# Optimization experiments

Hardware: AMD Instinct MI355X
Metric: run time of the kernel (lower is better)

Reference implementation:

```python
import jax, jax.numpy as jnp
import numpy as np

N_NODES = 50000
N_EDGES = 800000
IN_CH, HID, OUT_CH, EDGE_DIM = 256, 128, 64, 64
NUM_LAYERS = 3


def _linear_init(key, fan_in, fan_out):
    # torch nn.Linear default: U(-1/sqrt(fan_in), 1/sqrt(fan_in))
    kw, kb = jax.random.split(key)
    bound = 1.0 / np.sqrt(fan_in)
    W = jax.random.uniform(kw, (fan_in, fan_out), minval=-bound, maxval=bound, dtype=jnp.float32)
    b = jax.random.uniform(kb, (fan_out,), minval=-bound, maxval=bound, dtype=jnp.float32)
    return W, b


def setup_inputs() -> dict:
    key = jax.random.key(0)
    ks = jax.random.split(key, 8)
    x = jax.random.normal(ks[0], (N_NODES, IN_CH), dtype=jnp.float32)
    edge_index = jax.random.randint(ks[1], (2, N_EDGES), 0, N_NODES, dtype=jnp.int64)
    edge_attr = jax.random.normal(ks[2], (N_EDGES, EDGE_DIM), dtype=jnp.float32)
    W_in, b_in = _linear_init(ks[3], IN_CH, HID)
    W_e, b_e = _linear_init(ks[4], EDGE_DIM, HID)
    W1, b1 = _linear_init(ks[5], HID, HID)
    W2, b2 = _linear_init(ks[6], HID, HID)
    W_out, b_out = _linear_init(ks[7], HID, OUT_CH)
    return {"x": x, "edge_index": edge_index, "edge_attr": edge_attr,
            "W_in": W_in, "b_in": b_in, "W_e": W_e, "b_e": b_e,
            "W1": W1, "b1": b1, "W2": W2, "b2": b2,
            "W_out": W_out, "b_out": b_out}


def reference(x, edge_index, edge_attr, W_in, b_in, W_e, b_e, W1, b1, W2, b2, W_out, b_out):
    N = x.shape[0]
    src, dst = edge_index[0], edge_index[1]
    # input projection (in_channels != hidden_channels)
    h = x @ W_in + b_in                      # [N, HID]
    # edge projection is layer-independent (shared GINEConv weights)
    e = edge_attr @ W_e + b_e                # [E, HID]
    for _ in range(NUM_LAYERS):
        # GINEConv: message = relu(h_src + e), sum-aggregate to dst, eps=0
        msg = jax.nn.relu(h[src] + e)        # [E, HID]
        agg = jax.ops.segment_sum(msg, dst, num_segments=N)
        z = h + agg                          # (1+eps)*h + agg, eps=0
        # conv nn: MLP Linear->relu->Linear (plain_last)
        z = jax.nn.relu(z @ W1 + b1) @ W2 + b2
        # outer act
        h = jax.nn.relu(z)
    return h @ W_out + b_out                 # [N, OUT_CH]
```

## Files before the change

### kernel.cpp

```cpp
#include <hip/hip_runtime.h>
#include <hip/hip_bf16.h>
#include <stdint.h>

#define N_NODES 50000
#define N_EDGES 800000
#define IN_CH 256
#define HID 128
#define OUT_CH 64
#define EDGE_DIM 64

typedef __hip_bfloat16 bf16;
typedef __attribute__((ext_vector_type(8))) short short8;
typedef __attribute__((ext_vector_type(4))) float f32x4;

__device__ __forceinline__ void st_out(float* p, float v) { *p = v; }
__device__ __forceinline__ void st_out(bf16* p, float v) { *p = __float2bfloat16(v); }

__launch_bounds__(256)
__global__ void wt_prep(const float* __restrict__ W, bf16* __restrict__ Wt, int K, int N) {
    int i = blockIdx.x * 256 + threadIdx.x;
    if (i >= K * N) return;
    int n = i % N, k = i / N;
    Wt[n * K + k] = __float2bfloat16(W[i]);
}

template<int KTOT, int N, bool RELU, bool PERM, typename OutT>
__launch_bounds__(256)
__global__ void gemm_mfma(const float* __restrict__ A, const bf16* __restrict__ Wt,
                          const float* __restrict__ b, OutT* __restrict__ out,
                          int M, const int* __restrict__ operm) {
    constexpr int KC  = (KTOT >= 128) ? 128 : KTOT;
    constexpr int NCH = KTOT / KC;
    constexpr int KCP = KC + 8;
    constexpr int NT  = N / 16;
    __shared__ __align__(16) bf16 Ws[N * KCP];
    __shared__ __align__(16) bf16 As[64 * KCP];

    const int tid  = threadIdx.x;
    const int wave = tid >> 6;
    const int lane = tid & 63;
    const int quad = lane >> 4;
    const int l16  = lane & 15;
    const int base = blockIdx.x * 64;

    f32x4 acc[NT];
    #pragma unroll
    for (int i = 0; i < NT; i++) acc[i] = (f32x4){0.f, 0.f, 0.f, 0.f};

    for (int ch = 0; ch < NCH; ch++) {
        const int kc = ch * KC;
        for (int t = tid * 4; t < N * KC; t += 256 * 4) {
            int n = t / KC, k = t % KC;
            *(uint2*)&Ws[n * KCP + k] = *(const uint2*)&Wt[n * KTOT + kc + k];
        }
        for (int t = tid * 4; t < 64 * KC; t += 256 * 4) {
            int r = t / KC, k = t % KC;
            int gr = base + r;
            float4 v = (gr < M) ? *(const float4*)&A[(size_t)gr * KTOT + kc + k]
                                : make_float4(0.f, 0.f, 0.f, 0.f);
            __hip_bfloat162 p0 = __float22bfloat162_rn(make_float2(v.x, v.y));
            __hip_bfloat162 p1 = __float22bfloat162_rn(make_float2(v.z, v.w));
            *(__hip_bfloat162*)&As[r * KCP + k]     = p0;
            *(__hip_bfloat162*)&As[r * KCP + k + 2] = p1;
        }
        __syncthreads();

        const bf16* arow = &As[(wave * 16 + l16) * KCP];
        #pragma unroll
        for (int ks = 0; ks < KC / 32; ks++) {
            short8 af = *(const short8*)&arow[ks * 32 + quad * 8];
            #pragma unroll
            for (int nt = 0; nt < NT; nt++) {
                short8 bfr = *(const short8*)&Ws[(nt * 16 + l16) * KCP + ks * 32 + quad * 8];
                acc[nt] = __builtin_amdgcn_mfma_f32_16x16x32_bf16(af, bfr, acc[nt], 0, 0, 0);
            }
        }
        __syncthreads();
    }

    const int r0 = base + wave * 16 + quad * 4;
    #pragma unroll
    for (int reg = 0; reg < 4; reg++) {
        int gr = r0 + reg;
        if (gr < M) {
            int orow = PERM ? operm[gr] : gr;
            #pragma unroll
            for (int nt = 0; nt < NT; nt++) {
                int col = nt * 16 + l16;
                float v = acc[nt][reg] + b[col];
                if (RELU) v = fmaxf(v, 0.f);
                st_out(&out[(size_t)orow * N + col], v);
            }
        }
    }
}

__launch_bounds__(256)
__global__ void hist_kernel(const int* __restrict__ ei, int* __restrict__ counts) {
    int edge = blockIdx.x * 256 + threadIdx.x;
    if (edge < N_EDGES) atomicAdd(&counts[ei[N_EDGES + edge]], 1);
}

__launch_bounds__(1024)
__global__ void scan_kernel(const int* __restrict__ counts, int* __restrict__ offsets,
                            int* __restrict__ cursor) {
    __shared__ int part[1024];
    const int tid = threadIdx.x;
    const int CH = (N_NODES + 1023) / 1024;
    int beg = tid * CH, end = min(beg + CH, N_NODES);
    int s = 0;
    for (int i = beg; i < end; i++) s += counts[i];
    part[tid] = s;
    __syncthreads();
    for (int off = 1; off < 1024; off <<= 1) {
        int t = (tid >= off) ? part[tid - off] : 0;
        __syncthreads();
        part[tid] += t;
        __syncthreads();
    }
    int run = (tid == 0) ? 0 : part[tid - 1];
    for (int i = beg; i < end; i++) {
        offsets[i] = run;
        cursor[i] = run;
        run += counts[i];
    }
    if (tid == 1023) offsets[N_NODES] = part[1023];
}

__launch_bounds__(256)
__global__ void scatter_perm(const int* __restrict__ ei, int* __restrict__ cursor,
                             int* __restrict__ pos_of_edge, int* __restrict__ src_sorted) {
    int edge = blockIdx.x * 256 + threadIdx.x;
    if (edge >= N_EDGES) return;
    int dst = ei[N_EDGES + edge];
    int pos = atomicAdd(&cursor[dst], 1);
    pos_of_edge[edge] = pos;
    src_sorted[pos] = ei[edge];
}

__launch_bounds__(256)
__global__ void agg_kernel(const int* __restrict__ offsets, const int* __restrict__ src_sorted,
                           const bf16* __restrict__ e, const float* __restrict__ h,
                           float* __restrict__ z) {
    int wid = (blockIdx.x * 256 + threadIdx.x) >> 6;
    int lane = threadIdx.x & 63;
    if (wid >= N_NODES) return;
    int beg = offsets[wid], end = offsets[wid + 1];
    int c = lane * 2;
    float2 acc = {0.f, 0.f};
    int i = beg;
    for (; i + 1 < end; i += 2) {
        int s0 = src_sorted[i], s1 = src_sorted[i + 1];
        uint32_t ev0 = *(const uint32_t*)&e[i * HID + c];
        uint32_t ev1 = *(const uint32_t*)&e[(i + 1) * HID + c];
        float2 h0 = *(const float2*)&h[s0 * HID + c];
        float2 h1 = *(const float2*)&h[s1 * HID + c];
        acc.x += fmaxf(h0.x + __uint_as_float(ev0 << 16), 0.f);
        acc.y += fmaxf(h0.y + __uint_as_float(ev0 & 0xffff0000u), 0.f);
        acc.x += fmaxf(h1.x + __uint_as_float(ev1 << 16), 0.f);
        acc.y += fmaxf(h1.y + __uint_as_float(ev1 & 0xffff0000u), 0.f);
    }
    if (i < end) {
        int s0 = src_sorted[i];
        uint32_t ev0 = *(const uint32_t*)&e[i * HID + c];
        float2 h0 = *(const float2*)&h[s0 * HID + c];
        acc.x += fmaxf(h0.x + __uint_as_float(ev0 << 16), 0.f);
        acc.y += fmaxf(h0.y + __uint_as_float(ev0 & 0xffff0000u), 0.f);
    }
    float2 hv = *(const float2*)&h[wid * HID + c];
    acc.x += hv.x;
    acc.y += hv.y;
    *(float2*)&z[wid * HID + c] = acc;
}

extern "C" void kernel_launch(void* const* d_in, const int* in_sizes, int n_in,
                              void* d_out, int out_size, void* d_ws, size_t ws_size,
                              hipStream_t stream) {
    const float* x     = (const float*)d_in[0];
    const int*   ei    = (const int*)d_in[1];
    const float* ea    = (const float*)d_in[2];
    const float* W_in  = (const float*)d_in[3];
    const float* b_in  = (const float*)d_in[4];
    const float* W_e   = (const float*)d_in[5];
    const float* b_e   = (const float*)d_in[6];
    const float* W1    = (const float*)d_in[7];
    const float* b1    = (const float*)d_in[8];
    const float* W2    = (const float*)d_in[9];
    const float* b2    = (const float*)d_in[10];
    const float* W_out = (const float*)d_in[11];
    const float* b_out = (const float*)d_in[12];
    float* out = (float*)d_out;

    char* ws = (char*)d_ws;
    size_t off = 0;
    float* h       = (float*)(ws + off); off += (size_t)N_NODES * HID * 4;
    float* z       = (float*)(ws + off); off += (size_t)N_NODES * HID * 4;
    bf16*  e       = (bf16*) (ws + off); off += (size_t)N_EDGES * HID * 2;
    int*   counts  = (int*)  (ws + off); off += (size_t)N_NODES * 4;
    int*   offsets = (int*)  (ws + off); off += (size_t)(N_NODES + 1) * 4;
    int*   cursor  = (int*)  (ws + off); off += (size_t)N_NODES * 4;
    int*   poe     = (int*)  (ws + off); off += (size_t)N_EDGES * 4;
    int*   srcs    = (int*)  (ws + off); off += (size_t)N_EDGES * 4;
    bf16*  Wt_in   = (bf16*) (ws + off); off += (size_t)HID * IN_CH * 2;
    bf16*  Wt_e    = (bf16*) (ws + off); off += (size_t)HID * EDGE_DIM * 2;
    bf16*  Wt_1    = (bf16*) (ws + off); off += (size_t)HID * HID * 2;
    bf16*  Wt_2    = (bf16*) (ws + off); off += (size_t)HID * HID * 2;
    bf16*  Wt_out  = (bf16*) (ws + off); off += (size_t)OUT_CH * HID * 2;

    wt_prep<<<(IN_CH * HID + 255) / 256, 256, 0, stream>>>(W_in, Wt_in, IN_CH, HID);
    wt_prep<<<(EDGE_DIM * HID + 255) / 256, 256, 0, stream>>>(W_e, Wt_e, EDGE_DIM, HID);
    wt_prep<<<(HID * HID + 255) / 256, 256, 0, stream>>>(W1, Wt_1, HID, HID);
    wt_prep<<<(HID * HID + 255) / 256, 256, 0, stream>>>(W2, Wt_2, HID, HID);
    wt_prep<<<(HID * OUT_CH + 255) / 256, 256, 0, stream>>>(W_out, Wt_out, HID, OUT_CH);

    hipMemsetAsync(counts, 0, (size_t)N_NODES * 4, stream);
    hist_kernel<<<(N_EDGES + 255) / 256, 256, 0, stream>>>(ei, counts);
    scan_kernel<<<1, 1024, 0, stream>>>(counts, offsets, cursor);
    scatter_perm<<<(N_EDGES + 255) / 256, 256, 0, stream>>>(ei, cursor, poe, srcs);

    const int GN = (N_NODES + 63) / 64;
    const int GE = (N_EDGES + 63) / 64;

    gemm_mfma<IN_CH, HID, false, false, float>
        <<<GN, 256, 0, stream>>>(x, Wt_in, b_in, h, N_NODES, nullptr);

    gemm_mfma<EDGE_DIM, HID, false, true, bf16>
        <<<GE, 256, 0, stream>>>(ea, Wt_e, b_e, e, N_EDGES, poe);

    for (int layer = 0; layer < 3; ++layer) {
        agg_kernel<<<(N_NODES * 64 + 255) / 256, 256, 0, stream>>>(offsets, srcs, e, h, z);
        gemm_mfma<HID, HID, true, false, float>
            <<<GN, 256, 0, stream>>>(z, Wt_1, b1, h, N_NODES, nullptr);
        gemm_mfma<HID, HID, true, false, float>
            <<<GN, 256, 0, stream>>>(h, Wt_2, b2, z, N_NODES, nullptr);
        float* t = h; h = z; z = t;
    }

    gemm_mfma<HID, OUT_CH, false, false, float>
        <<<GN, 256, 0, stream>>>(h, Wt_out, b_out, out, N_NODES, nullptr);
}
```

Measured before the change: 1.047 ms.

## Store node activations in bf16, merge weight prep, retile GEMM with multi-row waves

Node features h and z are now stored as bf16 rather than fp32, which halves the gather traffic in the aggregation kernel and the GEMM input and output bandwidth. The GEMM gains an MROWS template parameter so the edge projection can process 128 rows per block, uses KC=64 chunks with 16-byte vector loads, and has a bf16-input path. The five weight-prep launches are merged into one kernel. The cost is reduced precision for the intermediate node activations across all three layers.

```diff
diff --git a/kernel.cpp b/kernel.cpp
--- a/kernel.cpp
+++ b/kernel.cpp
@@ -16,80 +16,116 @@
 __device__ __forceinline__ void st_out(float* p, float v) { *p = v; }
 __device__ __forceinline__ void st_out(bf16* p, float v) { *p = __float2bfloat16(v); }
 
-__launch_bounds__(256)
-__global__ void wt_prep(const float* __restrict__ W, bf16* __restrict__ Wt, int K, int N) {
-    int i = blockIdx.x * 256 + threadIdx.x;
-    if (i >= K * N) return;
+__device__ __forceinline__ void wt_one(const float* W, bf16* Wt, int K, int N, int i) {
     int n = i % N, k = i / N;
     Wt[n * K + k] = __float2bfloat16(W[i]);
 }
-
-template<int KTOT, int N, bool RELU, bool PERM, typename OutT>
-__launch_bounds__(256)
-__global__ void gemm_mfma(const float* __restrict__ A, const bf16* __restrict__ Wt,
+__launch_bounds__(256)
+__global__ void wt_prep_all(const float* W_in, const float* W_e, const float* W1,
+                            const float* W2, const float* W_out,
+                            bf16* Wt_in, bf16* Wt_e, bf16* Wt_1, bf16* Wt_2, bf16* Wt_out) {
+    int i = blockIdx.x * 256 + threadIdx.x;
+    if (i < 32768)       wt_one(W_in,  Wt_in,  256, 128, i);
+    else if (i < 40960)  wt_one(W_e,   Wt_e,    64, 128, i - 32768);
+    else if (i < 57344)  wt_one(W1,    Wt_1,   128, 128, i - 40960);
+    else if (i < 73728)  wt_one(W2,    Wt_2,   128, 128, i - 57344);
+    else if (i < 81920)  wt_one(W_out, Wt_out, 128,  64, i - 73728);
+}
+
+template<int KTOT, int N, int MROWS, bool RELU, bool PERM, typename InT, typename OutT>
+__launch_bounds__(256)
+__global__ void gemm_mfma(const InT* __restrict__ A, const bf16* __restrict__ Wt,
                           const float* __restrict__ b, OutT* __restrict__ out,
                           int M, const int* __restrict__ operm) {
-    constexpr int KC  = (KTOT >= 128) ? 128 : KTOT;
+    static_assert(KTOT % 64 == 0, "");
+    constexpr int KC  = 64;
     constexpr int NCH = KTOT / KC;
     constexpr int KCP = KC + 8;
     constexpr int NT  = N / 16;
+    constexpr int MT  = MROWS / 64;
     __shared__ __align__(16) bf16 Ws[N * KCP];
-    __shared__ __align__(16) bf16 As[64 * KCP];
+    __shared__ __align__(16) bf16 As[MROWS * KCP];
 
     const int tid  = threadIdx.x;
     const int wave = tid >> 6;
     const int lane = tid & 63;
     const int quad = lane >> 4;
     const int l16  = lane & 15;
-    const int base = blockIdx.x * 64;
-
-    f32x4 acc[NT];
+    const int base = blockIdx.x * MROWS;
+
+    f32x4 acc[MT][NT];
     #pragma unroll
-    for (int i = 0; i < NT; i++) acc[i] = (f32x4){0.f, 0.f, 0.f, 0.f};
+    for (int m = 0; m < MT; m++)
+        #pragma unroll
+        for (int i = 0; i < NT; i++) acc[m][i] = (f32x4){0.f, 0.f, 0.f, 0.f};
 
     for (int ch = 0; ch < NCH; ch++) {
         const int kc = ch * KC;
-        for (int t = tid * 4; t < N * KC; t += 256 * 4) {
-            int n = t / KC, k = t % KC;
-            *(uint2*)&Ws[n * KCP + k] = *(const uint2*)&Wt[n * KTOT + kc + k];
-        }
-        for (int t = tid * 4; t < 64 * KC; t += 256 * 4) {
-            int r = t / KC, k = t % KC;
-            int gr = base + r;
-            float4 v = (gr < M) ? *(const float4*)&A[(size_t)gr * KTOT + kc + k]
-                                : make_float4(0.f, 0.f, 0.f, 0.f);
-            __hip_bfloat162 p0 = __float22bfloat162_rn(make_float2(v.x, v.y));
-            __hip_bfloat162 p1 = __float22bfloat162_rn(make_float2(v.z, v.w));
-            *(__hip_bfloat162*)&As[r * KCP + k]     = p0;
-            *(__hip_bfloat162*)&As[r * KCP + k + 2] = p1;
-        }
-        __syncthreads();
-
-        const bf16* arow = &As[(wave * 16 + l16) * KCP];
+        constexpr int WIT = N * KC / (256 * 8);
+        #pragma unroll
+        for (int it = 0; it < WIT; it++) {
+            int t8 = (it * 256 + tid) * 8;
+            int n = t8 / KC, k = t8 % KC;
+            *(uint4*)&Ws[n * KCP + k] = *(const uint4*)&Wt[n * KTOT + kc + k];
+        }
+        if constexpr (sizeof(InT) == 4) {
+            constexpr int AIT = MROWS * KC / (256 * 4);
+            #pragma unroll
+            for (int it = 0; it < AIT; it++) {
+                int t4 = (it * 256 + tid) * 4;
+                int r = t4 / KC, k = t4 % KC;
+                int gr = base + r;
+                float4 v = (gr < M) ? *(const float4*)&A[(size_t)gr * KTOT + kc + k]
+                                    : make_float4(0.f, 0.f, 0.f, 0.f);
+                *(__hip_bfloat162*)&As[r * KCP + k]     = __float22bfloat162_rn(make_float2(v.x, v.y));
+                *(__hip_bfloat162*)&As[r * KCP + k + 2] = __float22bfloat162_rn(make_float2(v.z, v.w));
+            }
+        } else {
+            constexpr int AIT = MROWS * KC / (256 * 8);
+            #pragma unroll
+            for (int it = 0; it < AIT; it++) {
+                int t8 = (it * 256 + tid) * 8;
+                int r = t8 / KC, k = t8 % KC;
+                int gr = base + r;
+                uint4 v = (gr < M) ? *(const uint4*)&A[(size_t)gr * KTOT + kc + k]
+                                   : make_uint4(0u, 0u, 0u, 0u);
+                *(uint4*)&As[r * KCP + k] = v;
+            }
+        }
+        __syncthreads();
+
         #pragma unroll
         for (int ks = 0; ks < KC / 32; ks++) {
-            short8 af = *(const short8*)&arow[ks * 32 + quad * 8];
+            short8 af[MT];
+            #pragma unroll
+            for (int m = 0; m < MT; m++)
+                af[m] = *(const short8*)&As[(wave * MT * 16 + m * 16 + l16) * KCP + ks * 32 + quad * 8];
             #pragma unroll
             for (int nt = 0; nt < NT; nt++) {
                 short8 bfr = *(const short8*)&Ws[(nt * 16 + l16) * KCP + ks * 32 + quad * 8];
-                acc[nt] = __builtin_amdgcn_mfma_f32_16x16x32_bf16(af, bfr, acc[nt], 0, 0, 0);
-            }
-        }
-        __syncthreads();
-    }
-
-    const int r0 = base + wave * 16 + quad * 4;
+                #pragma unroll
+                for (int m = 0; m < MT; m++)
+                    acc[m][nt] = __builtin_amdgcn_mfma_f32_16x16x32_bf16(af[m], bfr, acc[m][nt], 0, 0, 0);
+            }
+        }
+        __syncthreads();
+    }
+
     #pragma unroll
-    for (int reg = 0; reg < 4; reg++) {
-        int gr = r0 + reg;
-        if (gr < M) {
-            int orow = PERM ? operm[gr] : gr;
-            #pragma unroll
-            for (int nt = 0; nt < NT; nt++) {
-                int col = nt * 16 + l16;
-                float v = acc[nt][reg] + b[col];
-                if (RELU) v = fmaxf(v, 0.f);
-                st_out(&out[(size_t)orow * N + col], v);
+    for (int m = 0; m < MT; m++) {
+        const int r0 = base + wave * MT * 16 + m * 16 + quad * 4;
+        #pragma unroll
+        for (int reg = 0; reg < 4; reg++) {
+            int gr = r0 + reg;
+            if (gr < M) {
+                int orow = PERM ? operm[gr] : gr;
+                #pragma unroll
+                for (int nt = 0; nt < NT; nt++) {
+                    int col = nt * 16 + l16;
+                    float v = acc[m][nt][reg] + b[col];
+                    if (RELU) v = fmaxf(v, 0.f);
+                    st_out(&out[(size_t)orow * N + col], v);
+                }
             }
         }
     }
@@ -138,10 +174,13 @@
     src_sorted[pos] = ei[edge];
 }
 
+__device__ __forceinline__ float blo(uint32_t u) { return __uint_as_float(u << 16); }
+__device__ __forceinline__ float bhi(uint32_t u) { return __uint_as_float(u & 0xffff0000u); }
+
 __launch_bounds__(256)
 __global__ void agg_kernel(const int* __restrict__ offsets, const int* __restrict__ src_sorted,
-                           const bf16* __restrict__ e, const float* __restrict__ h,
-                           float* __restrict__ z) {
+                           const bf16* __restrict__ e, const bf16* __restrict__ h,
+                           bf16* __restrict__ z) {
     int wid = (blockIdx.x * 256 + threadIdx.x) >> 6;
     int lane = threadIdx.x & 63;
     if (wid >= N_NODES) return;
@@ -153,24 +192,25 @@
         int s0 = src_sorted[i], s1 = src_sorted[i + 1];
         uint32_t ev0 = *(const uint32_t*)&e[i * HID + c];
         uint32_t ev1 = *(const uint32_t*)&e[(i + 1) * HID + c];
-        float2 h0 = *(const float2*)&h[s0 * HID + c];
-        float2 h1 = *(const float2*)&h[s1 * HID + c];
-        acc.x += fmaxf(h0.x + __uint_as_float(ev0 << 16), 0.f);
-        acc.y += fmaxf(h0.y + __uint_as_float(ev0 & 0xffff0000u), 0.f);
-        acc.x += fmaxf(h1.x + __uint_as_float(ev1 << 16), 0.f);
-        acc.y += fmaxf(h1.y + __uint_as_float(ev1 & 0xffff0000u), 0.f);
+        uint32_t h0 = *(const uint32_t*)&h[s0 * HID + c];
+        uint32_t h1 = *(const uint32_t*)&h[s1 * HID + c];
+        acc.x += fmaxf(blo(h0) + blo(ev0), 0.f);
+        acc.y += fmaxf(bhi(h0) + bhi(ev0), 0.f);
+        acc.x += fmaxf(blo(h1) + blo(ev1), 0.f);
+        acc.y += fmaxf(bhi(h1) + bhi(ev1), 0.f);
     }
     if (i < end) {
         int s0 = src_sorted[i];
         uint32_t ev0 = *(const uint32_t*)&e[i * HID + c];
-        float2 h0 = *(const float2*)&h[s0 * HID + c];
-        acc.x += fmaxf(h0.x + __uint_as_float(ev0 << 16), 0.f);
-        acc.y += fmaxf(h0.y + __uint_as_float(ev0 & 0xffff0000u), 0.f);
-    }
-    float2 hv = *(const float2*)&h[wid * HID + c];
-    acc.x += hv.x;
-    acc.y += hv.y;
-    *(float2*)&z[wid * HID + c] = acc;
+        uint32_t h0 = *(const uint32_t*)&h[s0 * HID + c];
+        acc.x += fmaxf(blo(h0) + blo(ev0), 0.f);
+        acc.y += fmaxf(bhi(h0) + bhi(ev0), 0.f);
+    }
+    uint32_t hs = *(const uint32_t*)&h[wid * HID + c];
+    acc.x += blo(hs);
+    acc.y += bhi(hs);
+    __hip_bfloat162 p = __float22bfloat162_rn(make_float2(acc.x, acc.y));
+    *(__hip_bfloat162*)&z[wid * HID + c] = p;
 }
 
 extern "C" void kernel_launch(void* const* d_in, const int* in_sizes, int n_in,
@@ -193,8 +233,8 @@
 
     char* ws = (char*)d_ws;
     size_t off = 0;
-    float* h       = (float*)(ws + off); off += (size_t)N_NODES * HID * 4;
-    float* z       = (float*)(ws + off); off += (size_t)N_NODES * HID * 4;
+    bf16*  h       = (bf16*) (ws + off); off += (size_t)N_NODES * HID * 2;
+    bf16*  z       = (bf16*) (ws + off); off += (size_t)N_NODES * HID * 2;
     bf16*  e       = (bf16*) (ws + off); off += (size_t)N_EDGES * HID * 2;
     int*   counts  = (int*)  (ws + off); off += (size_t)N_NODES * 4;
     int*   offsets = (int*)  (ws + off); off += (size_t)(N_NODES + 1) * 4;
@@ -207,35 +247,29 @@
     bf16*  Wt_2    = (bf16*) (ws + off); off += (size_t)HID * HID * 2;
     bf16*  Wt_out  = (bf16*) (ws + off); off += (size_t)OUT_CH * HID * 2;
 
-    wt_prep<<<(IN_CH * HID + 255) / 256, 256, 0, stream>>>(W_in, Wt_in, IN_CH, HID);
-    wt_prep<<<(EDGE_DIM * HID + 255) / 256, 256, 0, stream>>>(W_e, Wt_e, EDGE_DIM, HID);
-    wt_prep<<<(HID * HID + 255) / 256, 256, 0, stream>>>(W1, Wt_1, HID, HID);
-    wt_prep<<<(HID * HID + 255) / 256, 256, 0, stream>>>(W2, Wt_2, HID, HID);
-    wt_prep<<<(HID * OUT_CH + 255) / 256, 256, 0, stream>>>(W_out, Wt_out, HID, OUT_CH);
+    wt_prep_all<<<(81920 + 255) / 256, 256, 0, stream>>>(
+        W_in, W_e, W1, W2, W_out, Wt_in, Wt_e, Wt_1, Wt_2, Wt_out);
 
     hipMemsetAsync(counts, 0, (size_t)N_NODES * 4, stream);
     hist_kernel<<<(N_EDGES + 255) / 256, 256, 0, stream>>>(ei, counts);
     scan_kernel<<<1, 1024, 0, stream>>>(counts, offsets, cursor);
     scatter_perm<<<(N_EDGES + 255) / 256, 256, 0, stream>>>(ei, cursor, poe, srcs);
 
-    const int GN = (N_NODES + 63) / 64;
-    const int GE = (N_EDGES + 63) / 64;
-
-    gemm_mfma<IN_CH, HID, false, false, float>
-        <<<GN, 256, 0, stream>>>(x, Wt_in, b_in, h, N_NODES, nullptr);
-
-    gemm_mfma<EDGE_DIM, HID, false, true, bf16>
-        <<<GE, 256, 0, stream>>>(ea, Wt_e, b_e, e, N_EDGES, poe);
+    gemm_mfma<IN_CH, HID, 64, false, false, float, bf16>
+        <<<(N_NODES + 63) / 64, 256, 0, stream>>>(x, Wt_in, b_in, h, N_NODES, nullptr);
+
+    gemm_mfma<EDGE_DIM, HID, 128, false, true, float, bf16>
+        <<<(N_EDGES + 127) / 128, 256, 0, stream>>>(ea, Wt_e, b_e, e, N_EDGES, poe);
 
     for (int layer = 0; layer < 3; ++layer) {
         agg_kernel<<<(N_NODES * 64 + 255) / 256, 256, 0, stream>>>(offsets, srcs, e, h, z);
-        gemm_mfma<HID, HID, true, false, float>
-            <<<GN, 256, 0, stream>>>(z, Wt_1, b1, h, N_NODES, nullptr);
-        gemm_mfma<HID, HID, true, false, float>
-            <<<GN, 256, 0, stream>>>(h, Wt_2, b2, z, N_NODES, nullptr);
-        float* t = h; h = z; z = t;
-    }
-
-    gemm_mfma<HID, OUT_CH, false, false, float>
-        <<<GN, 256, 0, stream>>>(h, Wt_out, b_out, out, N_NODES, nullptr);
-}
+        gemm_mfma<HID, HID, 64, true, false, bf16, bf16>
+            <<<(N_NODES + 63) / 64, 256, 0, stream>>>(z, Wt_1, b1, h, N_NODES, nullptr);
+        gemm_mfma<HID, HID, 64, true, false, bf16, bf16>
+            <<<(N_NODES + 63) / 64, 256, 0, stream>>>(h, Wt_2, b2, z, N_NODES, nullptr);
+        bf16* t = h; h = z; z = t;
+    }
+
+    gemm_mfma<HID, OUT_CH, 64, false, false, bf16, float>
+        <<<(N_NODES + 63) / 64, 256, 0, stream>>>(h, Wt_out, b_out, out, N_NODES, nullptr);
+}
```

Measured after the change: 886.8 us. 1.18x faster.
